# Optimization experiments

Measured on AMD Instinct MI355X. Metric: run time of the kernel, lower is better.

Reference implementation:

```python
import jax, jax.numpy as jnp
import numpy as np

WINDOW_SIZE = 7
NB_HEADS = 8


def _relative_position_index(ws: int) -> np.ndarray:
    coords = np.stack(np.meshgrid(np.arange(ws), np.arange(ws), indexing='ij'))  # [2, ws, ws]
    flat = coords.reshape(2, -1)  # [2, ws*ws]
    rel = flat[:, :, None] - flat[:, None, :]  # [2, N, N]
    rel = rel.transpose(1, 2, 0)
    rel[:, :, 0] += ws - 1
    rel[:, :, 1] += ws - 1
    rel[:, :, 0] *= 2 * ws - 1
    return rel.sum(-1).astype(np.int64)  # [N, N]


def setup_inputs() -> dict:
    key = jax.random.key(0)
    ks = jax.random.split(key, 7)
    B_, N, C = 2048, WINDOW_SIZE * WINDOW_SIZE, 256
    nW = 64
    return {
        'x': jax.random.normal(ks[0], (B_, N, C), dtype=jnp.float32),
        'mask': jax.random.normal(ks[1], (nW, N, N), dtype=jnp.float32),
        'qkv_w': jax.random.normal(ks[2], (C, 3 * C), dtype=jnp.float32) * 0.02,
        'qkv_b': jax.random.normal(ks[3], (3 * C,), dtype=jnp.float32) * 0.02,
        'proj_w': jax.random.normal(ks[4], (C, C), dtype=jnp.float32) * 0.02,
        'proj_b': jax.random.normal(ks[5], (C,), dtype=jnp.float32) * 0.02,
        'bias_table': jax.random.normal(ks[6], ((2 * WINDOW_SIZE - 1) ** 2, NB_HEADS), dtype=jnp.float32) * 0.02,
    }


def reference(x, mask, qkv_w, qkv_b, proj_w, proj_b, bias_table):
    B_, N, C = x.shape
    h = NB_HEADS
    d = C // h
    rpi = jnp.asarray(_relative_position_index(WINDOW_SIZE))  # [N, N] int

    qkv = x @ qkv_w + qkv_b  # [B_, N, 3C]
    qkv = qkv.reshape(B_, N, 3, h, d).transpose(2, 0, 3, 1, 4)  # [3, B_, h, N, d]
    q, k, v = qkv[0], qkv[1], qkv[2]

    scale = d ** -0.5
    attn = jnp.einsum('bhnd,bhmd->bhnm', q * scale, k)  # [B_, h, N, N]

    # relative position bias gather: [N*N, h] -> [h, N, N]
    bias = bias_table[rpi.reshape(-1)].reshape(N, N, h).transpose(2, 0, 1)
    attn = attn + bias[None]

    nW = mask.shape[0]
    attn = attn.reshape(B_ // nW, nW, h, N, N) + mask[None, :, None]  # broadcast mask over heads
    attn = attn.reshape(B_, h, N, N)
    attn = jax.nn.softmax(attn, axis=-1)

    out = jnp.einsum('bhnm,bhmd->bhnd', attn, v)  # [B_, h, N, d]
    out = out.transpose(0, 2, 1, 3).reshape(B_, N, C)
    return out @ proj_w + proj_b
```

## Files before the change

### kernel.cpp

```cpp
#include <hip/hip_runtime.h>
#include <hip/hip_bf16.h>

typedef __attribute__((ext_vector_type(8))) short bf16x8;
typedef __attribute__((ext_vector_type(4))) float f32x4;

static __device__ __forceinline__ short b16(float f) {
    __hip_bfloat16 h = __float2bfloat16(f);
    return *reinterpret_cast<short*>(&h);
}

__global__ void k_prep(const float* __restrict__ qkv_w, const float* __restrict__ qkv_b,
                       const float* __restrict__ proj_w, const float* __restrict__ bias_table,
                       const float* __restrict__ mask,
                       __hip_bfloat16* __restrict__ qwT, __hip_bfloat16* __restrict__ pwT,
                       float* __restrict__ qb_s, float* __restrict__ cbt) {
    const float scale = 0.17677669529663687f;
    const int P1 = 768 * 256, P2 = P1 + 256 * 256, P3 = P2 + 768, P4 = P3 + 64 * 8 * 4 * 4 * 64;
    int i = blockIdx.x * 256 + threadIdx.x;
    if (i < P1) {
        int nc = i >> 8, kc = i & 255;
        float v = qkv_w[kc * 768 + nc];
        if (nc < 256) v *= scale;
        qwT[i] = __float2bfloat16(v);
    } else if (i < P2) {
        int j = i - P1;
        int nc = j >> 8, kc = j & 255;
        pwT[j] = __float2bfloat16(proj_w[kc * 256 + nc]);
    } else if (i < P3) {
        int j = i - P2;
        qb_s[j] = qkv_b[j] * (j < 256 ? scale : 1.f);
    } else if (i < P4) {
        int j = i - P3;
        int w = j >> 13;
        int h = (j >> 10) & 7;
        int rt = (j >> 8) & 3;
        int ct = (j >> 6) & 3;
        int lane = j & 63;
        int m = ct * 16 + (lane & 15);
        f32x4 v;
#pragma unroll
        for (int reg = 0; reg < 4; ++reg) {
            int n = rt * 16 + 4 * (lane >> 4) + reg;
            float val;
            if (m >= 49) val = -1e30f;
            else if (n >= 49) val = 0.f;
            else {
                int i1 = n / 7, j1 = n % 7, i2 = m / 7, j2 = m % 7;
                int rpi = (i1 - i2 + 6) * 13 + (j1 - j2 + 6);
                val = bias_table[rpi * 8 + h] + mask[(w * 49 + n) * 49 + m];
            }
            v[reg] = val;
        }
        ((f32x4*)cbt)[j] = v;
    }
}

#define XS_OFF    0
#define PL_OFF(h) ((h) * 6272)
#define QK_OFF    50176
#define QS(h)     (QK_OFF + (h) * 8000)
#define KS(h)     (QK_OFF + (h) * 8000 + 4000)
#define AS_OFF    QK_OFF
#define VT(h)     (114176 + (h) * 4608)
#define LDS_TOTAL 151040

__global__ __launch_bounds__(512, 2)
void win_fused(const float* __restrict__ x,
               const __hip_bfloat16* __restrict__ qwT,
               const __hip_bfloat16* __restrict__ pwT,
               const float* __restrict__ qb_s,
               const float* __restrict__ proj_b,
               const float* __restrict__ cbt,
               float* __restrict__ out) {
    __shared__ alignas(16) char lds[LDS_TOTAL];
    const int b = blockIdx.x;
    const int tid = threadIdx.x;
    const int h = tid >> 6, lane = tid & 63, g = lane >> 4, c0 = lane & 15;

    const float* xw = x + (size_t)b * 12544;
    for (int i = tid; i < 3136; i += 512) {
        int row = i >> 6, col4 = i & 63;
        float4 v = *(const float4*)(xw + row * 256 + col4 * 4);
        union { unsigned long long u; short s[4]; } o;
        o.s[0] = b16(v.x); o.s[1] = b16(v.y); o.s[2] = b16(v.z); o.s[3] = b16(v.w);
        int byte = row * 512 + (((col4 >> 1) ^ (row & 7)) << 4) + (col4 & 1) * 8;
        *(unsigned long long*)(lds + byte) = o.u;
    }
    __syncthreads();

    f32x4 acc[3][4][2];
#pragma unroll
    for (int q3 = 0; q3 < 3; ++q3)
#pragma unroll
        for (int rt = 0; rt < 4; ++rt)
#pragma unroll
            for (int ct2 = 0; ct2 < 2; ++ct2)
#pragma unroll
                for (int r = 0; r < 4; ++r) acc[q3][rt][ct2][r] = 0.f;

#pragma unroll
    for (int kt = 0; kt < 8; ++kt) {
        bf16x8 af[4];
#pragma unroll
        for (int rt = 0; rt < 4; ++rt) {
            int row = rt * 16 + c0;
            af[rt] = *(const bf16x8*)(lds + row * 512 + (((kt * 4 + g) ^ (c0 & 7)) << 4));
        }
#pragma unroll
        for (int q3 = 0; q3 < 3; ++q3) {
#pragma unroll
            for (int ct2 = 0; ct2 < 2; ++ct2) {
                bf16x8 bw = *(const bf16x8*)(qwT + (size_t)(q3 * 256 + h * 32 + ct2 * 16 + c0) * 256
                                             + kt * 32 + g * 8);
#pragma unroll
                for (int rt = 0; rt < 4; ++rt)
                    acc[q3][rt][ct2] = __builtin_amdgcn_mfma_f32_16x16x32_bf16(
                        af[rt], bw, acc[q3][rt][ct2], 0, 0, 0);
            }
        }
    }
#pragma unroll
    for (int q3 = 0; q3 < 3; ++q3) {
#pragma unroll
        for (int ct2 = 0; ct2 < 2; ++ct2) {
            float bias = qb_s[q3 * 256 + h * 32 + ct2 * 16 + c0];
            int d0 = ct2 * 16 + c0;
#pragma unroll
            for (int rt = 0; rt < 4; ++rt) {
#pragma unroll
                for (int reg = 0; reg < 4; ++reg) {
                    int n = rt * 16 + 4 * g + reg;
                    if (q3 == 2) {
                        short sv = (n < 49) ? b16(acc[q3][rt][ct2][reg] + bias) : (short)0;
                        *(short*)(lds + VT(h) + d0 * 144 + n * 2) = sv;
                    } else if (n < 49) {
                        short sv = b16(acc[q3][rt][ct2][reg] + bias);
                        if (q3 == 0) *(short*)(lds + QS(h) + n * 80 + d0 * 2) = sv;
                        else         *(short*)(lds + KS(h) + n * 80 + d0 * 2) = sv;
                    }
                }
            }
        }
    }
    __syncthreads();

    bf16x8 qf[4], kf[4];
#pragma unroll
    for (int t = 0; t < 4; ++t) {
        int n = t * 16 + c0;
        int nc = n < 49 ? n : 48;
        qf[t] = *(const bf16x8*)(lds + QS(h) + nc * 80 + g * 16);
        kf[t] = *(const bf16x8*)(lds + KS(h) + nc * 80 + g * 16);
    }
    const f32x4* cbb = (const f32x4*)cbt + ((size_t)((b & 63) * 8 + h)) * 1024;
    const f32x4 zf = {0.f, 0.f, 0.f, 0.f};

#pragma unroll
    for (int rt = 0; rt < 4; ++rt) {
        f32x4 cb[4];
#pragma unroll
        for (int ct = 0; ct < 4; ++ct) cb[ct] = cbb[(rt * 4 + ct) * 64 + lane];
        f32x4 s[4];
        __builtin_amdgcn_s_setprio(1);
#pragma unroll
        for (int ct = 0; ct < 4; ++ct)
            s[ct] = __builtin_amdgcn_mfma_f32_16x16x32_bf16(qf[rt], kf[ct], zf, 0, 0, 0);
        __builtin_amdgcn_s_setprio(0);
#pragma unroll
        for (int ct = 0; ct < 4; ++ct)
#pragma unroll
            for (int reg = 0; reg < 4; ++reg) s[ct][reg] += cb[ct][reg];
#pragma unroll
        for (int reg = 0; reg < 4; ++reg) {
            int n = rt * 16 + 4 * g + reg;
            float mx = fmaxf(fmaxf(s[0][reg], s[1][reg]), fmaxf(s[2][reg], s[3][reg]));
            mx = fmaxf(mx, __shfl_xor(mx, 1));
            mx = fmaxf(mx, __shfl_xor(mx, 2));
            mx = fmaxf(mx, __shfl_xor(mx, 4));
            mx = fmaxf(mx, __shfl_xor(mx, 8));
            float sum = 0.f;
#pragma unroll
            for (int ct = 0; ct < 4; ++ct) {
                float e = __expf(s[ct][reg] - mx);
                s[ct][reg] = e;
                sum += e;
            }
            sum += __shfl_xor(sum, 1);
            sum += __shfl_xor(sum, 2);
            sum += __shfl_xor(sum, 4);
            sum += __shfl_xor(sum, 8);
            float inv = 1.f / sum;
            if (n < 49) {
#pragma unroll
                for (int ct = 0; ct < 4; ++ct) {
                    int m = ct * 16 + c0;
                    int byte = (n * 128 + m * 2) ^ ((n & 7) << 4);
                    *(short*)(lds + PL_OFF(h) + byte) = b16(s[ct][reg] * inv);
                }
            }
        }
    }
    __syncthreads();

    f32x4 o[4][2];
#pragma unroll
    for (int rt = 0; rt < 4; ++rt)
#pragma unroll
        for (int ci = 0; ci < 2; ++ci)
#pragma unroll
            for (int r = 0; r < 4; ++r) o[rt][ci][r] = 0.f;
#pragma unroll
    for (int kt2 = 0; kt2 < 2; ++kt2) {
        bf16x8 pa[4], vb[2];
#pragma unroll
        for (int rt = 0; rt < 4; ++rt) {
            int row = rt * 16 + c0;
            int rc = row < 49 ? row : 48;
            int byte = rc * 128 + (((kt2 * 4 + g) ^ (rc & 7)) << 4);
            pa[rt] = *(const bf16x8*)(lds + PL_OFF(h) + byte);
        }
#pragma unroll
        for (int ci = 0; ci < 2; ++ci)
            vb[ci] = *(const bf16x8*)(lds + VT(h) + (ci * 16 + c0) * 144 + (kt2 * 32 + g * 8) * 2);
        __builtin_amdgcn_s_setprio(1);
#pragma unroll
        for (int rt = 0; rt < 4; ++rt)
#pragma unroll
            for (int ci = 0; ci < 2; ++ci)
                o[rt][ci] = __builtin_amdgcn_mfma_f32_16x16x32_bf16(pa[rt], vb[ci], o[rt][ci], 0, 0, 0);
        __builtin_amdgcn_s_setprio(0);
    }
#pragma unroll
    for (int rt = 0; rt < 4; ++rt) {
#pragma unroll
        for (int ci = 0; ci < 2; ++ci) {
#pragma unroll
            for (int reg = 0; reg < 4; ++reg) {
                int n = rt * 16 + 4 * g + reg;
                if (n < 49) {
                    int col = h * 32 + ci * 16 + c0;
                    *(short*)(lds + AS_OFF + n * 512 + (((col >> 3) ^ (n & 7)) << 4) + (col & 7) * 2)
                        = b16(o[rt][ci][reg]);
                }
            }
        }
    }
    __syncthreads();

    f32x4 po[4][2];
#pragma unroll
    for (int rt = 0; rt < 4; ++rt)
#pragma unroll
        for (int ct2 = 0; ct2 < 2; ++ct2)
#pragma unroll
            for (int r = 0; r < 4; ++r) po[rt][ct2][r] = 0.f;
#pragma unroll
    for (int kt = 0; kt < 8; ++kt) {
        bf16x8 paf[4], pb[2];
#pragma unroll
        for (int rt = 0; rt < 4; ++rt) {
            int row = rt * 16 + c0;
            paf[rt] = *(const bf16x8*)(lds + AS_OFF + row * 512 + (((kt * 4 + g) ^ (c0 & 7)) << 4));
        }
#pragma unroll
        for (int ct2 = 0; ct2 < 2; ++ct2)
            pb[ct2] = *(const bf16x8*)(pwT + (size_t)(h * 32 + ct2 * 16 + c0) * 256 + kt * 32 + g * 8);
#pragma unroll
        for (int rt = 0; rt < 4; ++rt)
#pragma unroll
            for (int ct2 = 0; ct2 < 2; ++ct2)
                po[rt][ct2] = __builtin_amdgcn_mfma_f32_16x16x32_bf16(
                    paf[rt], pb[ct2], po[rt][ct2], 0, 0, 0);
    }
    float* ob = out + (size_t)b * 12544;
    float pbias[2];
#pragma unroll
    for (int ct2 = 0; ct2 < 2; ++ct2) pbias[ct2] = proj_b[h * 32 + ct2 * 16 + c0];
#pragma unroll
    for (int rt = 0; rt < 4; ++rt) {
#pragma unroll
        for (int ct2 = 0; ct2 < 2; ++ct2) {
#pragma unroll
            for (int reg = 0; reg < 4; ++reg) {
                int n = rt * 16 + 4 * g + reg;
                if (n < 49)
                    ob[(size_t)n * 256 + h * 32 + ct2 * 16 + c0] = po[rt][ct2][reg] + pbias[ct2];
            }
        }
    }
}

extern "C" void kernel_launch(void* const* d_in, const int* in_sizes, int n_in,
                              void* d_out, int out_size, void* d_ws, size_t ws_size,
                              hipStream_t stream) {
    const float* x          = (const float*)d_in[0];
    const float* mask       = (const float*)d_in[1];
    const float* qkv_w      = (const float*)d_in[2];
    const float* qkv_b      = (const float*)d_in[3];
    const float* proj_w     = (const float*)d_in[4];
    const float* proj_b     = (const float*)d_in[5];
    const float* bias_table = (const float*)d_in[6];

    const int C = 256, NN = 49;
    const int M  = in_sizes[0] / C;
    const int B_ = M / NN;

    char* ws = (char*)d_ws;
    __hip_bfloat16* qwT = (__hip_bfloat16*)ws;
    size_t off = (size_t)768 * 256 * 2;
    __hip_bfloat16* pwT = (__hip_bfloat16*)(ws + off); off += (size_t)256 * 256 * 2;
    float* qb_s = (float*)(ws + off); off += (size_t)768 * 4;
    float* cbt  = (float*)(ws + off); off += (size_t)64 * 8 * 4096 * 4;

    int prep_total = 768 * 256 + 256 * 256 + 768 + 64 * 8 * 4 * 4 * 64;
    k_prep<<<(prep_total + 255) / 256, 256, 0, stream>>>(qkv_w, qkv_b, proj_w, bias_table, mask,
                                                         qwT, pwT, qb_s, cbt);
    win_fused<<<B_, 512, 0, stream>>>(x, qwT, pwT, qb_s, proj_b, cbt, (float*)d_out);
}
```

Before: 371.4 us.

## Keep Q/K/V in registers via transposed MFMA layouts and shrink LDS for occupancy

Computes Q and K with transposed MFMA operand order so the accumulator layout directly forms the bf16 operands for the QK^T MFMA, and packs V accumulators straight into PV B-operands. This removes the Q, K and V staging through shared memory and shrinks LDS from about 148KB to 49KB, letting launch bounds request four blocks per CU instead of two. The projection output buffer now reuses the x region, and row indices are clamped. More live registers per thread under the higher occupancy target could cause spills.

```diff
diff --git a/kernel.cpp b/kernel.cpp
--- a/kernel.cpp
+++ b/kernel.cpp
@@ -55,16 +55,10 @@
     }
 }
 
-#define XS_OFF    0
 #define PL_OFF(h) ((h) * 6272)
-#define QK_OFF    50176
-#define QS(h)     (QK_OFF + (h) * 8000)
-#define KS(h)     (QK_OFF + (h) * 8000 + 4000)
-#define AS_OFF    QK_OFF
-#define VT(h)     (114176 + (h) * 4608)
-#define LDS_TOTAL 151040
-
-__global__ __launch_bounds__(512, 2)
+#define LDS_TOTAL 50176
+
+__global__ __launch_bounds__(512, 4)
 void win_fused(const float* __restrict__ x,
                const __hip_bfloat16* __restrict__ qwT,
                const __hip_bfloat16* __restrict__ pwT,
@@ -88,73 +82,89 @@
     }
     __syncthreads();
 
-    f32x4 acc[3][4][2];
-#pragma unroll
-    for (int q3 = 0; q3 < 3; ++q3)
-#pragma unroll
-        for (int rt = 0; rt < 4; ++rt)
-#pragma unroll
-            for (int ct2 = 0; ct2 < 2; ++ct2)
-#pragma unroll
-                for (int r = 0; r < 4; ++r) acc[q3][rt][ct2][r] = 0.f;
-
+    const f32x4 zf = {0.f, 0.f, 0.f, 0.f};
+
+    f32x4 aq[2][4], ak[2][4];
+#pragma unroll
+    for (int dt = 0; dt < 2; ++dt)
+#pragma unroll
+        for (int nt = 0; nt < 4; ++nt) { aq[dt][nt] = zf; ak[dt][nt] = zf; }
 #pragma unroll
     for (int kt = 0; kt < 8; ++kt) {
         bf16x8 af[4];
 #pragma unroll
+        for (int nt = 0; nt < 4; ++nt) {
+            int row = nt * 16 + c0; int rc = row < 49 ? row : 48;
+            af[nt] = *(const bf16x8*)(lds + rc * 512 + (((kt * 4 + g) ^ (rc & 7)) << 4));
+        }
+#pragma unroll
+        for (int dt = 0; dt < 2; ++dt) {
+            bf16x8 wq = *(const bf16x8*)(qwT + (size_t)(h * 32 + dt * 16 + c0) * 256 + kt * 32 + g * 8);
+            bf16x8 wk = *(const bf16x8*)(qwT + (size_t)(256 + h * 32 + dt * 16 + c0) * 256 + kt * 32 + g * 8);
+#pragma unroll
+            for (int nt = 0; nt < 4; ++nt) {
+                aq[dt][nt] = __builtin_amdgcn_mfma_f32_16x16x32_bf16(wq, af[nt], aq[dt][nt], 0, 0, 0);
+                ak[dt][nt] = __builtin_amdgcn_mfma_f32_16x16x32_bf16(wk, af[nt], ak[dt][nt], 0, 0, 0);
+            }
+        }
+    }
+    bf16x8 qp[4], kp[4];
+    {
+        const float* qb = qb_s + h * 32 + 4 * g;
+        f32x4 qb0 = *(const f32x4*)(qb);
+        f32x4 qb1 = *(const f32x4*)(qb + 16);
+        f32x4 kb0 = *(const f32x4*)(qb + 256);
+        f32x4 kb1 = *(const f32x4*)(qb + 272);
+#pragma unroll
+        for (int nt = 0; nt < 4; ++nt) {
+#pragma unroll
+            for (int j = 0; j < 4; ++j) {
+                qp[nt][j]     = b16(aq[0][nt][j] + qb0[j]);
+                qp[nt][j + 4] = b16(aq[1][nt][j] + qb1[j]);
+                kp[nt][j]     = b16(ak[0][nt][j] + kb0[j]);
+                kp[nt][j + 4] = b16(ak[1][nt][j] + kb1[j]);
+            }
+        }
+    }
+
+    f32x4 av[4][2];
+#pragma unroll
+    for (int rt = 0; rt < 4; ++rt)
+#pragma unroll
+        for (int ci = 0; ci < 2; ++ci) av[rt][ci] = zf;
+#pragma unroll
+    for (int kt = 0; kt < 8; ++kt) {
+        bf16x8 af[4];
+#pragma unroll
         for (int rt = 0; rt < 4; ++rt) {
-            int row = rt * 16 + c0;
-            af[rt] = *(const bf16x8*)(lds + row * 512 + (((kt * 4 + g) ^ (c0 & 7)) << 4));
-        }
-#pragma unroll
-        for (int q3 = 0; q3 < 3; ++q3) {
-#pragma unroll
-            for (int ct2 = 0; ct2 < 2; ++ct2) {
-                bf16x8 bw = *(const bf16x8*)(qwT + (size_t)(q3 * 256 + h * 32 + ct2 * 16 + c0) * 256
-                                             + kt * 32 + g * 8);
-#pragma unroll
-                for (int rt = 0; rt < 4; ++rt)
-                    acc[q3][rt][ct2] = __builtin_amdgcn_mfma_f32_16x16x32_bf16(
-                        af[rt], bw, acc[q3][rt][ct2], 0, 0, 0);
-            }
-        }
-    }
-#pragma unroll
-    for (int q3 = 0; q3 < 3; ++q3) {
-#pragma unroll
-        for (int ct2 = 0; ct2 < 2; ++ct2) {
-            float bias = qb_s[q3 * 256 + h * 32 + ct2 * 16 + c0];
-            int d0 = ct2 * 16 + c0;
-#pragma unroll
-            for (int rt = 0; rt < 4; ++rt) {
-#pragma unroll
-                for (int reg = 0; reg < 4; ++reg) {
-                    int n = rt * 16 + 4 * g + reg;
-                    if (q3 == 2) {
-                        short sv = (n < 49) ? b16(acc[q3][rt][ct2][reg] + bias) : (short)0;
-                        *(short*)(lds + VT(h) + d0 * 144 + n * 2) = sv;
-                    } else if (n < 49) {
-                        short sv = b16(acc[q3][rt][ct2][reg] + bias);
-                        if (q3 == 0) *(short*)(lds + QS(h) + n * 80 + d0 * 2) = sv;
-                        else         *(short*)(lds + KS(h) + n * 80 + d0 * 2) = sv;
-                    }
-                }
-            }
-        }
+            int row = rt * 16 + c0; int rc = row < 49 ? row : 48;
+            af[rt] = *(const bf16x8*)(lds + rc * 512 + (((kt * 4 + g) ^ (rc & 7)) << 4));
+        }
+#pragma unroll
+        for (int ci = 0; ci < 2; ++ci) {
+            bf16x8 wv = *(const bf16x8*)(qwT + (size_t)(512 + h * 32 + ci * 16 + c0) * 256 + kt * 32 + g * 8);
+#pragma unroll
+            for (int rt = 0; rt < 4; ++rt)
+                av[rt][ci] = __builtin_amdgcn_mfma_f32_16x16x32_bf16(af[rt], wv, av[rt][ci], 0, 0, 0);
+        }
+    }
+    bf16x8 vp[2][2];
+    {
+        float vb0 = qb_s[512 + h * 32 + c0];
+        float vb1 = qb_s[512 + h * 32 + 16 + c0];
+#pragma unroll
+        for (int kt2 = 0; kt2 < 2; ++kt2)
+#pragma unroll
+            for (int j = 0; j < 4; ++j) {
+                vp[kt2][0][j]     = b16(av[2 * kt2][0][j] + vb0);
+                vp[kt2][0][j + 4] = b16(av[2 * kt2 + 1][0][j] + vb0);
+                vp[kt2][1][j]     = b16(av[2 * kt2][1][j] + vb1);
+                vp[kt2][1][j + 4] = b16(av[2 * kt2 + 1][1][j] + vb1);
+            }
     }
     __syncthreads();
 
-    bf16x8 qf[4], kf[4];
-#pragma unroll
-    for (int t = 0; t < 4; ++t) {
-        int n = t * 16 + c0;
-        int nc = n < 49 ? n : 48;
-        qf[t] = *(const bf16x8*)(lds + QS(h) + nc * 80 + g * 16);
-        kf[t] = *(const bf16x8*)(lds + KS(h) + nc * 80 + g * 16);
-    }
     const f32x4* cbb = (const f32x4*)cbt + ((size_t)((b & 63) * 8 + h)) * 1024;
-    const f32x4 zf = {0.f, 0.f, 0.f, 0.f};
-
 #pragma unroll
     for (int rt = 0; rt < 4; ++rt) {
         f32x4 cb[4];
@@ -164,7 +174,7 @@
         __builtin_amdgcn_s_setprio(1);
 #pragma unroll
         for (int ct = 0; ct < 4; ++ct)
-            s[ct] = __builtin_amdgcn_mfma_f32_16x16x32_bf16(qf[rt], kf[ct], zf, 0, 0, 0);
+            s[ct] = __builtin_amdgcn_mfma_f32_16x16x32_bf16(qp[rt], kp[ct], zf, 0, 0, 0);
         __builtin_amdgcn_s_setprio(0);
 #pragma unroll
         for (int ct = 0; ct < 4; ++ct)
@@ -200,36 +210,35 @@
             }
         }
     }
+
+    f32x4 o[4][2];
+#pragma unroll
+    for (int rt = 0; rt < 4; ++rt)
+#pragma unroll
+        for (int ci = 0; ci < 2; ++ci) o[rt][ci] = zf;
+#pragma unroll
+    for (int kt2 = 0; kt2 < 2; ++kt2) {
+        bf16x8 pa[4];
+#pragma unroll
+        for (int rt = 0; rt < 4; ++rt) {
+            int n = rt * 16 + c0; int rc = n < 49 ? n : 48;
+            int blo = (rc * 128 + 64 * kt2 + 8 * g) ^ ((rc & 7) << 4);
+            int bhi = (rc * 128 + 64 * kt2 + 32 + 8 * g) ^ ((rc & 7) << 4);
+            union { bf16x8 v; unsigned long long u[2]; } pu;
+            pu.u[0] = *(const unsigned long long*)(lds + PL_OFF(h) + blo);
+            pu.u[1] = *(const unsigned long long*)(lds + PL_OFF(h) + bhi);
+            pa[rt] = pu.v;
+        }
+        __builtin_amdgcn_s_setprio(1);
+#pragma unroll
+        for (int rt = 0; rt < 4; ++rt)
+#pragma unroll
+            for (int ci = 0; ci < 2; ++ci)
+                o[rt][ci] = __builtin_amdgcn_mfma_f32_16x16x32_bf16(pa[rt], vp[kt2][ci], o[rt][ci], 0, 0, 0);
+        __builtin_amdgcn_s_setprio(0);
+    }
     __syncthreads();
 
-    f32x4 o[4][2];
-#pragma unroll
-    for (int rt = 0; rt < 4; ++rt)
-#pragma unroll
-        for (int ci = 0; ci < 2; ++ci)
-#pragma unroll
-            for (int r = 0; r < 4; ++r) o[rt][ci][r] = 0.f;
-#pragma unroll
-    for (int kt2 = 0; kt2 < 2; ++kt2) {
-        bf16x8 pa[4], vb[2];
-#pragma unroll
-        for (int rt = 0; rt < 4; ++rt) {
-            int row = rt * 16 + c0;
-            int rc = row < 49 ? row : 48;
-            int byte = rc * 128 + (((kt2 * 4 + g) ^ (rc & 7)) << 4);
-            pa[rt] = *(const bf16x8*)(lds + PL_OFF(h) + byte);
-        }
-#pragma unroll
-        for (int ci = 0; ci < 2; ++ci)
-            vb[ci] = *(const bf16x8*)(lds + VT(h) + (ci * 16 + c0) * 144 + (kt2 * 32 + g * 8) * 2);
-        __builtin_amdgcn_s_setprio(1);
-#pragma unroll
-        for (int rt = 0; rt < 4; ++rt)
-#pragma unroll
-            for (int ci = 0; ci < 2; ++ci)
-                o[rt][ci] = __builtin_amdgcn_mfma_f32_16x16x32_bf16(pa[rt], vb[ci], o[rt][ci], 0, 0, 0);
-        __builtin_amdgcn_s_setprio(0);
-    }
 #pragma unroll
     for (int rt = 0; rt < 4; ++rt) {
 #pragma unroll
@@ -239,7 +248,7 @@
                 int n = rt * 16 + 4 * g + reg;
                 if (n < 49) {
                     int col = h * 32 + ci * 16 + c0;
-                    *(short*)(lds + AS_OFF + n * 512 + (((col >> 3) ^ (n & 7)) << 4) + (col & 7) * 2)
+                    *(short*)(lds + n * 512 + (((col >> 3) ^ (n & 7)) << 4) + (col & 7) * 2)
                         = b16(o[rt][ci][reg]);
                 }
             }
@@ -251,16 +260,14 @@
 #pragma unroll
     for (int rt = 0; rt < 4; ++rt)
 #pragma unroll
-        for (int ct2 = 0; ct2 < 2; ++ct2)
-#pragma unroll
-            for (int r = 0; r < 4; ++r) po[rt][ct2][r] = 0.f;
+        for (int ct2 = 0; ct2 < 2; ++ct2) po[rt][ct2] = zf;
 #pragma unroll
     for (int kt = 0; kt < 8; ++kt) {
         bf16x8 paf[4], pb[2];
 #pragma unroll
         for (int rt = 0; rt < 4; ++rt) {
-            int row = rt * 16 + c0;
-            paf[rt] = *(const bf16x8*)(lds + AS_OFF + row * 512 + (((kt * 4 + g) ^ (c0 & 7)) << 4));
+            int row = rt * 16 + c0; int rc = row < 49 ? row : 48;
+            paf[rt] = *(const bf16x8*)(lds + rc * 512 + (((kt * 4 + g) ^ (rc & 7)) << 4));
         }
 #pragma unroll
         for (int ct2 = 0; ct2 < 2; ++ct2)
```

Result: slower. 645.1 us (+73.7%).
